# Optimization experiments

Measured on AMD Instinct MI355X. Metric: run time of the kernel, lower is better.

## Reference

```python
import jax, jax.numpy as jnp
import numpy as np

V, H, HALF, L, B = 32000, 512, 256, 1024, 64
LN_EPS = 1e-5
DELTA_EPS = 1e-6


def _forward(seq, embed, ff_w1, ff_b1, ff_w2, ff_b2, ln_g, ln_b,
             sem_w, sem_b, epi_w, epi_b, out_w, out_b):
    # Encoder: embed -> residual FFN -> LayerNorm
    e = embed[seq]                                   # (B, L, H)
    ff = jax.nn.relu(e @ ff_w1 + ff_b1) @ ff_w2 + ff_b2
    x = e + ff
    mu = jnp.mean(x, axis=-1, keepdims=True)
    var = jnp.mean((x - mu) ** 2, axis=-1, keepdims=True)
    h = (x - mu) / jnp.sqrt(var + LN_EPS) * ln_g + ln_b  # (B, L, H)

    # Project all timesteps at once (batched GEMM instead of per-step Linear)
    ks_all = h @ sem_w + sem_b                       # (B, L, half)
    ke_all = h @ epi_w + epi_b                       # (B, L, half)

    Bsz = seq.shape[0]
    Ls = seq.shape[1]
    w_t = jnp.arange(1, Ls, dtype=h.dtype) / Ls      # (L-1,) linear recency weights

    def step(carry, inp):
        M_s, M_e = carry
        k_s, k_e, w = inp                            # (B, half), (B, half), scalar
        vps = jnp.einsum('bij,bj->bi', M_s, k_s)
        dvs = k_s - vps / (jnp.sum(k_s * k_s, axis=-1, keepdims=True) + DELTA_EPS)
        M_s = M_s + dvs[:, :, None] * k_s[:, None, :]
        vpe = jnp.einsum('bij,bj->bi', M_e, k_e)
        dve = k_e - vpe / (jnp.sum(k_e * k_e, axis=-1, keepdims=True) + DELTA_EPS)
        M_e = M_e + w * (dve[:, :, None] * k_e[:, None, :])
        return (M_s, M_e), None

    M0 = jnp.zeros((Bsz, HALF, HALF), dtype=h.dtype)
    xs = (jnp.swapaxes(ks_all[:, :-1], 0, 1),        # (L-1, B, half)
          jnp.swapaxes(ke_all[:, :-1], 0, 1),
          w_t)
    (M_s, M_e), _ = jax.lax.scan(step, (M0, M0), xs)

    cs = jnp.einsum('bij,bj->bi', M_s, ks_all[:, -1])
    ce = jnp.einsum('bij,bj->bi', M_e, ke_all[:, -1])
    return jnp.concatenate([cs, ce], axis=-1) @ out_w + out_b  # (B, V)


def setup_inputs() -> dict:
    key = jax.random.key(0)
    ks = jax.random.split(key, 8)
    n = lambda k, shape, s=0.02: jax.random.normal(k, shape, jnp.float32) * s
    return {
        'seq': jax.random.randint(ks[0], (B, L), 0, V),
        'embed': n(ks[1], (V, H)),
        'ff_w1': n(ks[2], (H, 2 * H)), 'ff_b1': jnp.zeros((2 * H,), jnp.float32),
        'ff_w2': n(ks[3], (2 * H, H)), 'ff_b2': jnp.zeros((H,), jnp.float32),
        'ln_g': jnp.ones((H,), jnp.float32), 'ln_b': jnp.zeros((H,), jnp.float32),
        'sem_w': n(ks[4], (H, HALF)), 'sem_b': jnp.zeros((HALF,), jnp.float32),
        'epi_w': n(ks[5], (H, HALF)), 'epi_b': jnp.zeros((HALF,), jnp.float32),
        'out_w': n(ks[6], (2 * HALF, V)), 'out_b': jnp.zeros((V,), jnp.float32),
    }


def reference(seq, embed, ff_w1, ff_b1, ff_w2, ff_b2, ln_g, ln_b,
              sem_w, sem_b, epi_w, epi_b, out_w, out_b):
    return _forward(seq, embed, ff_w1, ff_b1, ff_w2, ff_b2, ln_g, ln_b,
                    sem_w, sem_b, epi_w, epi_b, out_w, out_b)
```

## Files before the change

### kernel.cpp

```cpp
#include <hip/hip_runtime.h>

typedef unsigned short ushort_t;
typedef unsigned int uint_t;
typedef __attribute__((ext_vector_type(8))) short short8;
typedef __attribute__((ext_vector_type(4))) float f32x4;

static constexpr int V = 32000, H = 512, HALFD = 256, LSEQ = 1024, BB = 64;

__device__ __forceinline__ ushort_t f2bf(float f) {
    uint_t u = __float_as_uint(f);
    u = (u + 0x7FFFu + ((u >> 16) & 1u)) >> 16;
    return (ushort_t)u;
}
__device__ __forceinline__ float bf2f(ushort_t u) {
    return __uint_as_float(((uint_t)u) << 16);
}
__device__ __forceinline__ float bflo(uint_t u) { return __uint_as_float(u << 16); }
__device__ __forceinline__ float bfhi(uint_t u) { return __uint_as_float(u & 0xffff0000u); }

__global__ void transpose_cvt(const float* __restrict__ W, ushort_t* __restrict__ Wt,
                              int K, int N) {
    __shared__ float tile[32][33];
    int k0 = blockIdx.y * 32, n0 = blockIdx.x * 32;
    int tx = threadIdx.x & 31, ty = threadIdx.x >> 5;
    #pragma unroll
    for (int i = 0; i < 32; i += 8)
        tile[ty + i][tx] = W[(size_t)(k0 + ty + i) * N + n0 + tx];
    __syncthreads();
    #pragma unroll
    for (int i = 0; i < 32; i += 8)
        Wt[(size_t)(n0 + ty + i) * K + k0 + tx] = f2bf(tile[tx][ty + i]);
}

__global__ __launch_bounds__(256) void gemm_ffn1(
        const int* __restrict__ seqp, const float* __restrict__ embed,
        const ushort_t* __restrict__ Bt, const float* __restrict__ bias,
        ushort_t* __restrict__ Cout, int N, int K) {
    __shared__ __align__(16) ushort_t Al[128][40];
    __shared__ __align__(16) ushort_t Bl[128][40];
    int t = threadIdx.x;
    int m0 = blockIdx.y * 128, n0 = blockIdx.x * 128;
    int lane = t & 63, wid = t >> 6;
    int wm = (wid & 1) * 64, wn = (wid >> 1) * 64;
    int lid = lane & 15, quad = lane >> 4;
    int srow = t >> 2, skq = (t & 3) * 8;

    int tok0 = seqp[m0 + srow];
    int tok1 = seqp[m0 + 64 + srow];
    const float* e0 = embed + (size_t)tok0 * H + skq;
    const float* e1 = embed + (size_t)tok1 * H + skq;

    f32x4 acc[4][4];
    #pragma unroll
    for (int i = 0; i < 4; ++i)
        #pragma unroll
        for (int j = 0; j < 4; ++j)
            acc[i][j] = (f32x4){0.f, 0.f, 0.f, 0.f};

    for (int k0 = 0; k0 < K; k0 += 32) {
        float4 ea0 = *(const float4*)(e0 + k0);
        float4 eb0 = *(const float4*)(e0 + k0 + 4);
        float4 ea1 = *(const float4*)(e1 + k0);
        float4 eb1 = *(const float4*)(e1 + k0 + 4);
        short8 b0 = *(const short8*)(Bt + (size_t)(n0 + srow) * K + k0 + skq);
        short8 b1 = *(const short8*)(Bt + (size_t)(n0 + 64 + srow) * K + k0 + skq);
        short8 s0, s1;
        s0[0] = (short)f2bf(ea0.x); s0[1] = (short)f2bf(ea0.y);
        s0[2] = (short)f2bf(ea0.z); s0[3] = (short)f2bf(ea0.w);
        s0[4] = (short)f2bf(eb0.x); s0[5] = (short)f2bf(eb0.y);
        s0[6] = (short)f2bf(eb0.z); s0[7] = (short)f2bf(eb0.w);
        s1[0] = (short)f2bf(ea1.x); s1[1] = (short)f2bf(ea1.y);
        s1[2] = (short)f2bf(ea1.z); s1[3] = (short)f2bf(ea1.w);
        s1[4] = (short)f2bf(eb1.x); s1[5] = (short)f2bf(eb1.y);
        s1[6] = (short)f2bf(eb1.z); s1[7] = (short)f2bf(eb1.w);
        __syncthreads();
        *(short8*)&Al[srow][skq]      = s0;
        *(short8*)&Al[64 + srow][skq] = s1;
        *(short8*)&Bl[srow][skq]      = b0;
        *(short8*)&Bl[64 + srow][skq] = b1;
        __syncthreads();
        short8 af[4], bfr[4];
        #pragma unroll
        for (int i = 0; i < 4; ++i)
            af[i] = *(const short8*)&Al[wm + i * 16 + lid][quad * 8];
        #pragma unroll
        for (int i = 0; i < 4; ++i)
            bfr[i] = *(const short8*)&Bl[wn + i * 16 + lid][quad * 8];
        #pragma unroll
        for (int mt = 0; mt < 4; ++mt)
            #pragma unroll
            for (int nt = 0; nt < 4; ++nt)
                acc[mt][nt] = __builtin_amdgcn_mfma_f32_16x16x32_bf16(
                    af[mt], bfr[nt], acc[mt][nt], 0, 0, 0);
    }
    #pragma unroll
    for (int mt = 0; mt < 4; ++mt)
        #pragma unroll
        for (int nt = 0; nt < 4; ++nt)
            #pragma unroll
            for (int rg = 0; rg < 4; ++rg) {
                int row = m0 + wm + mt * 16 + quad * 4 + rg;
                int col = n0 + wn + nt * 16 + lid;
                float v = fmaxf(acc[mt][nt][rg] + bias[col], 0.f);
                Cout[(size_t)row * N + col] = f2bf(v);
            }
}

__global__ __launch_bounds__(256) void gemm_ffn2(
        const ushort_t* __restrict__ A, const ushort_t* __restrict__ Bt,
        const float* __restrict__ bias, const int* __restrict__ seqp,
        const float* __restrict__ embed, ushort_t* __restrict__ Cout,
        int N, int K) {
    __shared__ __align__(16) ushort_t Al[128][40];
    __shared__ __align__(16) ushort_t Bl[128][40];
    int t = threadIdx.x;
    int m0 = blockIdx.y * 128, n0 = blockIdx.x * 128;
    int lane = t & 63, wid = t >> 6;
    int wm = (wid & 1) * 64, wn = (wid >> 1) * 64;
    int lid = lane & 15, quad = lane >> 4;
    int srow = t >> 2, skq = (t & 3) * 8;

    f32x4 acc[4][4];
    #pragma unroll
    for (int i = 0; i < 4; ++i)
        #pragma unroll
        for (int j = 0; j < 4; ++j)
            acc[i][j] = (f32x4){0.f, 0.f, 0.f, 0.f};

    for (int k0 = 0; k0 < K; k0 += 32) {
        short8 a0 = *(const short8*)(A + (size_t)(m0 + srow) * K + k0 + skq);
        short8 a1 = *(const short8*)(A + (size_t)(m0 + 64 + srow) * K + k0 + skq);
        short8 b0 = *(const short8*)(Bt + (size_t)(n0 + srow) * K + k0 + skq);
        short8 b1 = *(const short8*)(Bt + (size_t)(n0 + 64 + srow) * K + k0 + skq);
        __syncthreads();
        *(short8*)&Al[srow][skq]      = a0;
        *(short8*)&Al[64 + srow][skq] = a1;
        *(short8*)&Bl[srow][skq]      = b0;
        *(short8*)&Bl[64 + srow][skq] = b1;
        __syncthreads();
        short8 af[4], bfr[4];
        #pragma unroll
        for (int i = 0; i < 4; ++i)
            af[i] = *(const short8*)&Al[wm + i * 16 + lid][quad * 8];
        #pragma unroll
        for (int i = 0; i < 4; ++i)
            bfr[i] = *(const short8*)&Bl[wn + i * 16 + lid][quad * 8];
        #pragma unroll
        for (int mt = 0; mt < 4; ++mt)
            #pragma unroll
            for (int nt = 0; nt < 4; ++nt)
                acc[mt][nt] = __builtin_amdgcn_mfma_f32_16x16x32_bf16(
                    af[mt], bfr[nt], acc[mt][nt], 0, 0, 0);
    }
    #pragma unroll
    for (int mt = 0; mt < 4; ++mt)
        #pragma unroll
        for (int rg = 0; rg < 4; ++rg) {
            int row = m0 + wm + mt * 16 + quad * 4 + rg;
            int tok = seqp[row];
            const float* erow = embed + (size_t)tok * H;
            #pragma unroll
            for (int nt = 0; nt < 4; ++nt) {
                int col = n0 + wn + nt * 16 + lid;
                float v = acc[mt][nt][rg] + bias[col] + erow[col];
                Cout[(size_t)row * N + col] = f2bf(v);
            }
        }
}

__global__ __launch_bounds__(256) void gemm_proj(
        const ushort_t* __restrict__ A, const ushort_t* __restrict__ Bt,
        const float* __restrict__ biasS, const float* __restrict__ biasE,
        ushort_t* __restrict__ outS, ushort_t* __restrict__ outE, int K) {
    __shared__ __align__(16) ushort_t Al[128][40];
    __shared__ __align__(16) ushort_t Bl[128][40];
    int t = threadIdx.x;
    int m0 = blockIdx.y * 128, n0 = blockIdx.x * 128;
    int lane = t & 63, wid = t >> 6;
    int wm = (wid & 1) * 64, wn = (wid >> 1) * 64;
    int lid = lane & 15, quad = lane >> 4;
    int srow = t >> 2, skq = (t & 3) * 8;

    f32x4 acc[4][4];
    #pragma unroll
    for (int i = 0; i < 4; ++i)
        #pragma unroll
        for (int j = 0; j < 4; ++j)
            acc[i][j] = (f32x4){0.f, 0.f, 0.f, 0.f};

    for (int k0 = 0; k0 < K; k0 += 32) {
        short8 a0 = *(const short8*)(A + (size_t)(m0 + srow) * K + k0 + skq);
        short8 a1 = *(const short8*)(A + (size_t)(m0 + 64 + srow) * K + k0 + skq);
        short8 b0 = *(const short8*)(Bt + (size_t)(n0 + srow) * K + k0 + skq);
        short8 b1 = *(const short8*)(Bt + (size_t)(n0 + 64 + srow) * K + k0 + skq);
        __syncthreads();
        *(short8*)&Al[srow][skq]      = a0;
        *(short8*)&Al[64 + srow][skq] = a1;
        *(short8*)&Bl[srow][skq]      = b0;
        *(short8*)&Bl[64 + srow][skq] = b1;
        __syncthreads();
        short8 af[4], bfr[4];
        #pragma unroll
        for (int i = 0; i < 4; ++i)
            af[i] = *(const short8*)&Al[wm + i * 16 + lid][quad * 8];
        #pragma unroll
        for (int i = 0; i < 4; ++i)
            bfr[i] = *(const short8*)&Bl[wn + i * 16 + lid][quad * 8];
        #pragma unroll
        for (int mt = 0; mt < 4; ++mt)
            #pragma unroll
            for (int nt = 0; nt < 4; ++nt)
                acc[mt][nt] = __builtin_amdgcn_mfma_f32_16x16x32_bf16(
                    af[mt], bfr[nt], acc[mt][nt], 0, 0, 0);
    }
    #pragma unroll
    for (int mt = 0; mt < 4; ++mt)
        #pragma unroll
        for (int nt = 0; nt < 4; ++nt)
            #pragma unroll
            for (int rg = 0; rg < 4; ++rg) {
                int row = m0 + wm + mt * 16 + quad * 4 + rg;
                int col = n0 + wn + nt * 16 + lid;
                if (col < 256)
                    outS[(size_t)row * HALFD + col] = f2bf(acc[mt][nt][rg] + biasS[col]);
                else
                    outE[(size_t)row * HALFD + col - 256] =
                        f2bf(acc[mt][nt][rg] + biasE[col - 256]);
            }
}

__global__ void ln_kernel(ushort_t* X, const float* __restrict__ g,
                          const float* __restrict__ bta) {
    int row = blockIdx.x * 4 + (threadIdx.x >> 6);
    int lane = threadIdx.x & 63;
    ushort_t* xr = X + (size_t)row * H + lane * 8;
    short8 xv = *(short8*)xr;
    float x[8];
    #pragma unroll
    for (int j = 0; j < 8; ++j) x[j] = bf2f((ushort_t)xv[j]);
    float s = 0.f, ss = 0.f;
    #pragma unroll
    for (int j = 0; j < 8; ++j) { s += x[j]; ss += x[j] * x[j]; }
    #pragma unroll
    for (int d = 1; d < 64; d <<= 1) { s += __shfl_xor(s, d); ss += __shfl_xor(ss, d); }
    float mu = s * (1.f / 512.f);
    float var = ss * (1.f / 512.f) - mu * mu;
    float rstd = rsqrtf(var + 1e-5f);
    float4 g0 = *(const float4*)(g + lane * 8);
    float4 g1 = *(const float4*)(g + lane * 8 + 4);
    float4 b0 = *(const float4*)(bta + lane * 8);
    float4 b1 = *(const float4*)(bta + lane * 8 + 4);
    float gg[8] = {g0.x, g0.y, g0.z, g0.w, g1.x, g1.y, g1.z, g1.w};
    float bb[8] = {b0.x, b0.y, b0.z, b0.w, b1.x, b1.y, b1.z, b1.w};
    short8 o;
    #pragma unroll
    for (int j = 0; j < 8; ++j)
        o[j] = (short)f2bf((x[j] - mu) * rstd * gg[j] + bb[j]);
    *(short8*)xr = o;
}

__global__ void beta_kernel(const ushort_t* __restrict__ k, float* __restrict__ beta) {
    int row = blockIdx.x * 4 + (threadIdx.x >> 6);
    int lane = threadIdx.x & 63;
    ushort4 a = *(const ushort4*)(k + (size_t)row * HALFD + lane * 4);
    float ax = bf2f(a.x), ay = bf2f(a.y), az = bf2f(a.z), aw = bf2f(a.w);
    float s = ax * ax + ay * ay + az * az + aw * aw;
    #pragma unroll
    for (int d = 1; d < 64; d <<= 1) s += __shfl_xor(s, d);
    if (lane == 0) beta[row] = s + 1e-6f;
}

__global__ __launch_bounds__(256) void tinv_kernel(
        const ushort_t* __restrict__ ks, const ushort_t* __restrict__ ke,
        const float* __restrict__ beta_s, const float* __restrict__ beta_e,
        ushort_t* __restrict__ Dg) {
    int blk = blockIdx.x;
    int ch = blk & 15;
    int bm = blk >> 4;
    int mat = bm & 1, b = bm >> 1;
    const ushort_t* Kp = (mat ? ke : ks) + ((size_t)b * LSEQ + ch * 64) * HALFD;
    const float* Bp = (mat ? beta_e : beta_s) + (size_t)b * LSEQ + ch * 64;

    __shared__ __align__(16) ushort_t Kl[64][264];
    __shared__ float Lm[64][65];
    __shared__ float Drow[64];
    __shared__ float betsl[64];

    int t = threadIdx.x;
    int lane = t & 63, wv = t >> 6;
    int lid = lane & 15, quad = lane >> 4;

    {
        int j = t >> 2, c0 = (t & 3) * 64;
        const ushort_t* src = Kp + (size_t)j * HALFD + c0;
        #pragma unroll
        for (int x = 0; x < 8; ++x)
            *(short8*)&Kl[j][c0 + x * 8] = *(const short8*)(src + x * 8);
    }
    if (t < 64) betsl[t] = Bp[t];
    __syncthreads();

    f32x4 g[4];
    #pragma unroll
    for (int i = 0; i < 4; ++i) g[i] = (f32x4){0.f, 0.f, 0.f, 0.f};
    #pragma unroll
    for (int kc = 0; kc < 8; ++kc) {
        short8 af = *(const short8*)&Kl[wv * 16 + lid][kc * 32 + quad * 8];
        #pragma unroll
        for (int nt = 0; nt < 4; ++nt) {
            short8 bq = *(const short8*)&Kl[nt * 16 + lid][kc * 32 + quad * 8];
            g[nt] = __builtin_amdgcn_mfma_f32_16x16x32_bf16(af, bq, g[nt], 0, 0, 0);
        }
    }
    const float invL = 1.0f / 1024.0f;
    #pragma unroll
    for (int nt = 0; nt < 4; ++nt)
        #pragma unroll
        for (int rg = 0; rg < 4; ++rg) {
            int i = wv * 16 + quad * 4 + rg;
            int j = nt * 16 + lid;
            int s = ch * 64 + i;
            float wgt = mat ? (float)(s + 1) * invL : 1.0f;
            if (s >= 1023) wgt = 0.f;
            float wb = wgt / betsl[i];
            Lm[i][j] = (j < i) ? g[nt][rg] * wb : 0.f;
        }
    __syncthreads();

    float a[16];
    #pragma unroll
    for (int ii = 0; ii < 16; ++ii) a[ii] = -Lm[wv * 16 + ii][lane];
    #pragma unroll 63
    for (int j = 0; j < 63; ++j) {
        if (wv == (j >> 4)) Drow[lane] = a[j & 15];
        __syncthreads();
        float dj = Drow[lane];
        #pragma unroll
        for (int ii = 0; ii < 16; ++ii) {
            int i = wv * 16 + ii;
            if (i > j) a[ii] -= Lm[i][j] * dj;
        }
        __syncthreads();
    }
    #pragma unroll
    for (int ii = 0; ii < 16; ++ii)
        Dg[(size_t)blk * 4096 + (size_t)(wv * 16 + ii) * 64 + lane] = f2bf(a[ii]);
}

__global__ __launch_bounds__(512) void scan_kernel(
        const ushort_t* __restrict__ ks, const ushort_t* __restrict__ ke,
        const float* __restrict__ beta_s, const float* __restrict__ beta_e,
        const ushort_t* __restrict__ Dg, float* __restrict__ c) {
    int blk = blockIdx.x;
    int b = blk >> 2, mat = (blk >> 1) & 1, half = blk & 1;
    const ushort_t* Kp = (mat ? ke : ks) + (size_t)b * LSEQ * HALFD;
    const float* Bp = (mat ? beta_e : beta_s) + (size_t)b * LSEQ;
    const ushort_t* Dp = Dg + (size_t)(b * 2 + mat) * 16 * 4096;

    __shared__ __align__(16) ushort_t Kl[64][264];
    __shared__ __align__(16) ushort_t MK[33792];
    __shared__ __align__(16) ushort_t RHSl[128][72];
    __shared__ __align__(16) ushort_t Ul[128][72];
    __shared__ __align__(16) ushort_t Dl[64][72];
    __shared__ float bets[LSEQ];

    ushort_t (*Ml)[264] = (ushort_t(*)[264])MK;
    ushort_t (*Kt)[72]  = (ushort_t(*)[72])MK;

    int t = threadIdx.x;
    int lane = t & 63, wid = t >> 6;
    int lid = lane & 15, quad = lane >> 4;
    int wm  = (wid & 1) * 64, wn  = (wid >> 1) * 64;
    int wm1 = (wid & 1) * 64, wn1 = (wid >> 1) * 16;

    #pragma unroll
    for (int i = 0; i < 2; ++i) bets[t + i * 512] = Bp[t + i * 512];

    f32x4 acc[4][4];
    #pragma unroll
    for (int i = 0; i < 4; ++i)
        #pragma unroll
        for (int j = 0; j < 4; ++j)
            acc[i][j] = (f32x4){0.f, 0.f, 0.f, 0.f};

    int sj = t >> 3, scb = (t & 7) * 8;
    short8 pf[4];
    {
        const ushort_t* kr = Kp + (size_t)sj * HALFD + scb;
        #pragma unroll
        for (int x = 0; x < 4; ++x) pf[x] = *(const short8*)(kr + x * 64);
    }
    short8 dpf = *(const short8*)(Dp + t * 8);
    const float invL = 1.0f / 1024.0f;

    for (int ch = 0; ch < 16; ++ch) {
        __syncthreads();
        #pragma unroll
        for (int x = 0; x < 4; ++x) *(short8*)&Kl[sj][scb + x * 64] = pf[x];
        *(short8*)&Dl[t >> 3][(t & 7) * 8] = dpf;
        #pragma unroll
        for (int mt = 0; mt < 4; ++mt)
            #pragma unroll
            for (int nt = 0; nt < 4; ++nt)
                #pragma unroll
                for (int rg = 0; rg < 4; ++rg)
                    Ml[wm + mt * 16 + quad * 4 + rg][wn + nt * 16 + lid] =
                        f2bf(acc[mt][nt][rg]);
        int nch = (ch + 1 < 16) ? ch + 1 : 15;
        {
            const ushort_t* kr = Kp + ((size_t)nch * 64 + sj) * HALFD + scb;
            #pragma unroll
            for (int x = 0; x < 4; ++x) pf[x] = *(const short8*)(kr + x * 64);
            dpf = *(const short8*)(Dp + (size_t)nch * 4096 + t * 8);
        }
        __syncthreads();

        f32x4 p0[4];
        #pragma unroll
        for (int i = 0; i < 4; ++i) p0[i] = (f32x4){0.f, 0.f, 0.f, 0.f};
        #pragma unroll
        for (int kc = 0; kc < 8; ++kc) {
            short8 bq = *(const short8*)&Kl[wn1 + lid][kc * 32 + quad * 8];
            #pragma unroll
            for (int mt = 0; mt < 4; ++mt) {
                short8 aq = *(const short8*)&Ml[wm1 + mt * 16 + lid][kc * 32 + quad * 8];
                p0[mt] = __builtin_amdgcn_mfma_f32_16x16x32_bf16(aq, bq, p0[mt], 0, 0, 0);
            }
        }
        __syncthreads();
        #pragma unroll
        for (int mt = 0; mt < 4; ++mt)
            #pragma unroll
            for (int nt = 0; nt < 4; ++nt)
                #pragma unroll
                for (int rg = 0; rg < 4; ++rg) {
                    float v = acc[mt][nt][rg];
                    Ml[wm + mt * 16 + quad * 4 + rg][wn + nt * 16 + lid] =
                        f2bf(v - bf2f(f2bf(v)));
                }
        __syncthreads();
        #pragma unroll
        for (int kc = 0; kc < 8; ++kc) {
            short8 bq = *(const short8*)&Kl[wn1 + lid][kc * 32 + quad * 8];
            #pragma unroll
            for (int mt = 0; mt < 4; ++mt) {
                short8 aq = *(const short8*)&Ml[wm1 + mt * 16 + lid][kc * 32 + quad * 8];
                p0[mt] = __builtin_amdgcn_mfma_f32_16x16x32_bf16(aq, bq, p0[mt], 0, 0, 0);
            }
        }
        int iB = wn1 + lid;
        int s = ch * 64 + iB;
        float wgt = mat ? (float)(s + 1) * invL : 1.0f;
        if (s >= 1023) wgt = 0.f;
        float wb = wgt / bets[s];
        float rhsf[4][4];
        #pragma unroll
        for (int mt = 0; mt < 4; ++mt)
            #pragma unroll
            for (int rg = 0; rg < 4; ++rg) {
                int r = wm1 + mt * 16 + quad * 4 + rg;
                float kv = bf2f(Kl[iB][half * 128 + r]);
                float rv = wgt * kv - wb * p0[mt][rg];
                rhsf[mt][rg] = rv;
                RHSl[r][iB] = f2bf(rv);
            }
        __syncthreads();

        {
            int c0 = wid * 32;
            #pragma unroll
            for (int rr = 0; rr < 4; ++rr) {
                short8 kv8 = *(const short8*)&Kl[lane][c0 + rr * 8];
                #pragma unroll
                for (int x = 0; x < 8; ++x)
                    Kt[c0 + rr * 8 + x][lane] = (ushort_t)kv8[x];
            }
        }
        f32x4 uf[4];
        #pragma unroll
        for (int i = 0; i < 4; ++i) uf[i] = (f32x4){0.f, 0.f, 0.f, 0.f};
        #pragma unroll
        for (int kc = 0; kc < 2; ++kc) {
            short8 bq = *(const short8*)&Dl[wn1 + lid][kc * 32 + quad * 8];
            #pragma unroll
            for (int mt = 0; mt < 4; ++mt) {
                short8 aq = *(const short8*)&RHSl[wm1 + mt * 16 + lid][kc * 32 + quad * 8];
                uf[mt] = __builtin_amdgcn_mfma_f32_16x16x32_bf16(aq, bq, uf[mt], 0, 0, 0);
            }
        }
        #pragma unroll
        for (int mt = 0; mt < 4; ++mt)
            #pragma unroll
            for (int rg = 0; rg < 4; ++rg) {
                int r = wm1 + mt * 16 + quad * 4 + rg;
                Ul[r][wn1 + lid] = f2bf(uf[mt][rg] + rhsf[mt][rg]);
            }
        __syncthreads();
        #pragma unroll
        for (int kc = 0; kc < 2; ++kc) {
            short8 bq4[4];
            #pragma unroll
            for (int nt = 0; nt < 4; ++nt)
                bq4[nt] = *(const short8*)&Kt[wn + nt * 16 + lid][kc * 32 + quad * 8];
            #pragma unroll
            for (int mt = 0; mt < 4; ++mt) {
                short8 aq = *(const short8*)&Ul[wm + mt * 16 + lid][kc * 32 + quad * 8];
                #pragma unroll
                for (int nt = 0; nt < 4; ++nt)
                    acc[mt][nt] = __builtin_amdgcn_mfma_f32_16x16x32_bf16(
                        aq, bq4[nt], acc[mt][nt], 0, 0, 0);
            }
        }
        __syncthreads();
        #pragma unroll
        for (int mt = 0; mt < 4; ++mt)
            #pragma unroll
            for (int rg = 0; rg < 4; ++rg) {
                int r = wm1 + mt * 16 + quad * 4 + rg;
                float u = uf[mt][rg] + rhsf[mt][rg];
                Ul[r][wn1 + lid] = f2bf(u - bf2f(f2bf(u)));
            }
        __syncthreads();
        #pragma unroll
        for (int kc = 0; kc < 2; ++kc) {
            short8 bq4[4];
            #pragma unroll
            for (int nt = 0; nt < 4; ++nt)
                bq4[nt] = *(const short8*)&Kt[wn + nt * 16 + lid][kc * 32 + quad * 8];
            #pragma unroll
            for (int mt = 0; mt < 4; ++mt) {
                short8 aq = *(const short8*)&Ul[wm + mt * 16 + lid][kc * 32 + quad * 8];
                #pragma unroll
                for (int nt = 0; nt < 4; ++nt)
                    acc[mt][nt] = __builtin_amdgcn_mfma_f32_16x16x32_bf16(
                        aq, bq4[nt], acc[mt][nt], 0, 0, 0);
            }
        }
    }

    __syncthreads();
    float* vsc = (float*)RHSl;
    float kvv[4];
    #pragma unroll
    for (int nt = 0; nt < 4; ++nt)
        kvv[nt] = bf2f(Kl[63][wn + nt * 16 + lid]);
    #pragma unroll
    for (int mt = 0; mt < 4; ++mt)
        #pragma unroll
        for (int rg = 0; rg < 4; ++rg) {
            float p = acc[mt][0][rg] * kvv[0] + acc[mt][1][rg] * kvv[1]
                    + acc[mt][2][rg] * kvv[2] + acc[mt][3][rg] * kvv[3];
            p += __shfl_xor(p, 1); p += __shfl_xor(p, 2);
            p += __shfl_xor(p, 4); p += __shfl_xor(p, 8);
            if (lid == 0)
                vsc[(wid >> 1) * 128 + wm + mt * 16 + quad * 4 + rg] = p;
        }
    __syncthreads();
    if (t < 128) {
        float sum = vsc[t] + vsc[128 + t] + vsc[256 + t] + vsc[384 + t];
        c[(size_t)b * 512 + mat * 256 + half * 128 + t] = sum;
    }
}

__global__ __launch_bounds__(512) void out_gemm(
        const float* __restrict__ c, const float* __restrict__ W,
        const float* __restrict__ bias, float* __restrict__ out) {
    __shared__ __align__(16) float cl[16][512];
    int t = threadIdx.x;
    int lane = t & 63, w = t >> 6;
    int cb = blockIdx.x * 256;
    int rb = blockIdx.y * 16;

    #pragma unroll
    for (int i = 0; i < 4; ++i) {
        int idx = t + i * 512;
        int row = idx >> 7, c4 = (idx & 127) * 4;
        *(float4*)&cl[row][c4] = *(const float4*)(c + (size_t)(rb + row) * 512 + c4);
    }
    __syncthreads();

    const float* wp = W + cb + lane * 4;
    int r0 = w * 2;
    f32x4 a0 = (f32x4){0.f, 0.f, 0.f, 0.f};
    f32x4 a1 = (f32x4){0.f, 0.f, 0.f, 0.f};

    #pragma unroll 2
    for (int k = 0; k < 512; k += 4) {
        f32x4 w0 = *(const f32x4*)(wp + (size_t)(k + 0) * V);
        f32x4 w1 = *(const f32x4*)(wp + (size_t)(k + 1) * V);
        f32x4 w2 = *(const f32x4*)(wp + (size_t)(k + 2) * V);
        f32x4 w3 = *(const f32x4*)(wp + (size_t)(k + 3) * V);
        f32x4 ca = *(const f32x4*)&cl[r0][k];
        f32x4 cb4 = *(const f32x4*)&cl[r0 + 1][k];
        a0 += ca[0] * w0; a0 += ca[1] * w1; a0 += ca[2] * w2; a0 += ca[3] * w3;
        a1 += cb4[0] * w0; a1 += cb4[1] * w1; a1 += cb4[2] * w2; a1 += cb4[3] * w3;
    }
    f32x4 bv = *(const f32x4*)(bias + cb + lane * 4);
    *(f32x4*)(out + (size_t)(rb + r0) * V + cb + lane * 4) = a0 + bv;
    *(f32x4*)(out + (size_t)(rb + r0 + 1) * V + cb + lane * 4) = a1 + bv;
}

extern "C" void kernel_launch(void* const* d_in, const int* in_sizes, int n_in,
                              void* d_out, int out_size, void* d_ws, size_t ws_size,
                              hipStream_t stream) {
    const int*   seq    = (const int*)d_in[0];
    const float* embed  = (const float*)d_in[1];
    const float* ff_w1  = (const float*)d_in[2];
    const float* ff_b1  = (const float*)d_in[3];
    const float* ff_w2  = (const float*)d_in[4];
    const float* ff_b2  = (const float*)d_in[5];
    const float* ln_g   = (const float*)d_in[6];
    const float* ln_b   = (const float*)d_in[7];
    const float* sem_w  = (const float*)d_in[8];
    const float* sem_b  = (const float*)d_in[9];
    const float* epi_w  = (const float*)d_in[10];
    const float* epi_b  = (const float*)d_in[11];
    const float* out_w  = (const float*)d_in[12];
    const float* out_b  = (const float*)d_in[13];
    float* outp = (float*)d_out;

    const int ML = BB * LSEQ;
    int RCH;
    if      (ws_size >= 271712256ull) RCH = 65536;
    else if (ws_size >= 120717312ull) RCH = 16384;
    else                              RCH = 8192;

    char* w = (char*)d_ws;
    size_t off = 0;
    ushort_t* ks_bf = (ushort_t*)(w + off); off += 33554432;
    ushort_t* ke_bf = (ushort_t*)(w + off); off += 33554432;
    ushort_t* ebc   = (ushort_t*)(w + off); off += (size_t)RCH * 512 * 2;
    ushort_t* t1c   = (ushort_t*)(w + off); off += (size_t)RCH * 1024 * 2;
    ushort_t* w1t   = (ushort_t*)(w + off); off += 1048576;
    ushort_t* w2t   = (ushort_t*)(w + off); off += 1048576;
    ushort_t* semt  = (ushort_t*)(w + off); off += 262144;
    ushort_t* epit  = (ushort_t*)(w + off); off += 262144;
    float*    bet_s = (float*)(w + off);    off += 262144;
    float*    bet_e = (float*)(w + off);    off += 262144;
    float*    cbuf  = (float*)(w + off);    off += 131072;
    ushort_t* Dbuf  = ebc;
    (void)t1c;

    transpose_cvt<<<dim3(1024 / 32, 512 / 32), 256, 0, stream>>>(ff_w1, w1t, 512, 1024);
    transpose_cvt<<<dim3(512 / 32, 1024 / 32), 256, 0, stream>>>(ff_w2, w2t, 1024, 512);
    transpose_cvt<<<dim3(256 / 32, 512 / 32), 256, 0, stream>>>(sem_w, semt, 512, 256);
    transpose_cvt<<<dim3(256 / 32, 512 / 32), 256, 0, stream>>>(epi_w, epit, 512, 256);

    for (int cc = 0; cc < ML / RCH; ++cc) {
        int c0 = cc * RCH;
        gemm_ffn1<<<dim3(1024 / 128, RCH / 128), 256, 0, stream>>>(
            seq + c0, embed, w1t, ff_b1, t1c, 1024, 512);
        gemm_ffn2<<<dim3(512 / 128, RCH / 128), 256, 0, stream>>>(
            t1c, w2t, ff_b2, seq + c0, embed, ebc, 512, 1024);
        ln_kernel<<<RCH / 4, 256, 0, stream>>>(ebc, ln_g, ln_b);
        gemm_proj<<<dim3(512 / 128, RCH / 128), 256, 0, stream>>>(
            ebc, semt, sem_b, epi_b,
            ks_bf + (size_t)c0 * HALFD, ke_bf + (size_t)c0 * HALFD, 512);
    }

    beta_kernel<<<ML / 4, 256, 0, stream>>>(ks_bf, bet_s);
    beta_kernel<<<ML / 4, 256, 0, stream>>>(ke_bf, bet_e);

    tinv_kernel<<<2048, 256, 0, stream>>>(ks_bf, ke_bf, bet_s, bet_e, Dbuf);
    scan_kernel<<<256, 512, 0, stream>>>(ks_bf, ke_bf, bet_s, bet_e, Dbuf, cbuf);

    out_gemm<<<dim3(125, 4), 512, 0, stream>>>(cbuf, out_w, out_b, outp);
}
```

Measured before the change: 1.006 ms.

## Barrier-free per-wave triangular inverse and paired DPP bf16 LDS stores in scan

Measured after the change: 961.9 us. -4.4%, faster.

```diff
diff --git a/kernel.cpp b/kernel.cpp
--- a/kernel.cpp
+++ b/kernel.cpp
@@ -17,6 +17,21 @@
 }
 __device__ __forceinline__ float bflo(uint_t u) { return __uint_as_float(u << 16); }
 __device__ __forceinline__ float bfhi(uint_t u) { return __uint_as_float(u & 0xffff0000u); }
+__device__ __forceinline__ float bfres(float v) { return v - bf2f(f2bf(v)); }
+
+__device__ __forceinline__ uint_t dppswap1(uint_t x) {
+    return (uint_t)__builtin_amdgcn_mov_dpp((int)x, 0xB1, 0xF, 0xF, true);
+}
+
+__device__ __forceinline__ void st_pair4(ushort_t* p0, int pitch, int codd,
+                                         float v0, float v1, float v2, float v3) {
+    uint_t b0 = f2bf(v0), b1 = f2bf(v1), b2 = f2bf(v2), b3 = f2bf(v3);
+    uint_t q0 = dppswap1(b0), q1 = dppswap1(b1), q2 = dppswap1(b2), q3 = dppswap1(b3);
+    uint_t wa = codd ? ((uint_t)q2 | ((uint_t)b2 << 16)) : ((uint_t)b0 | ((uint_t)q0 << 16));
+    uint_t wb = codd ? ((uint_t)q3 | ((uint_t)b3 << 16)) : ((uint_t)b1 | ((uint_t)q1 << 16));
+    *(uint_t*)(p0) = wa;
+    *(uint_t*)(p0 + pitch) = wb;
+}
 
 __global__ void transpose_cvt(const float* __restrict__ W, ushort_t* __restrict__ Wt,
                               int K, int N) {
@@ -274,77 +289,84 @@
         const ushort_t* __restrict__ ks, const ushort_t* __restrict__ ke,
         const float* __restrict__ beta_s, const float* __restrict__ beta_e,
         ushort_t* __restrict__ Dg) {
-    int blk = blockIdx.x;
-    int ch = blk & 15;
-    int bm = blk >> 4;
-    int mat = bm & 1, b = bm >> 1;
-    const ushort_t* Kp = (mat ? ke : ks) + ((size_t)b * LSEQ + ch * 64) * HALFD;
-    const float* Bp = (mat ? beta_e : beta_s) + (size_t)b * LSEQ + ch * 64;
-
-    __shared__ __align__(16) ushort_t Kl[64][264];
-    __shared__ float Lm[64][65];
-    __shared__ float Drow[64];
-    __shared__ float betsl[64];
+    __shared__ __align__(16) ushort_t Kl[64][280];
+    __shared__ __align__(16) ushort_t LmT[4][64][66];
+    __shared__ float betsl[4][64];
 
     int t = threadIdx.x;
     int lane = t & 63, wv = t >> 6;
     int lid = lane & 15, quad = lane >> 4;
-
-    {
-        int j = t >> 2, c0 = (t & 3) * 64;
-        const ushort_t* src = Kp + (size_t)j * HALFD + c0;
-        #pragma unroll
-        for (int x = 0; x < 8; ++x)
-            *(short8*)&Kl[j][c0 + x * 8] = *(const short8*)(src + x * 8);
-    }
-    if (t < 64) betsl[t] = Bp[t];
+    int blk0 = blockIdx.x * 4;
+    const float invL = 1.0f / 1024.0f;
+
+    for (int pp = 0; pp < 4; ++pp) {
+        int p = blk0 + pp;
+        int ch = p & 15, bm = p >> 4;
+        int mat = bm & 1, b = bm >> 1;
+        const ushort_t* Kp = (mat ? ke : ks) + ((size_t)b * LSEQ + ch * 64) * HALFD;
+        const float* Bp = (mat ? beta_e : beta_s) + (size_t)b * LSEQ + ch * 64;
+
+        __syncthreads();
+        {
+            int j = t >> 2, c0 = (t & 3) * 64;
+            const ushort_t* src = Kp + (size_t)j * HALFD + c0;
+            #pragma unroll
+            for (int x = 0; x < 8; ++x)
+                *(short8*)&Kl[j][c0 + x * 8] = *(const short8*)(src + x * 8);
+        }
+        if (t < 64) betsl[pp][t] = Bp[t];
+        __syncthreads();
+
+        f32x4 g[4];
+        #pragma unroll
+        for (int i = 0; i < 4; ++i) g[i] = (f32x4){0.f, 0.f, 0.f, 0.f};
+        #pragma unroll
+        for (int kc = 0; kc < 8; ++kc) {
+            short8 af = *(const short8*)&Kl[wv * 16 + lid][kc * 32 + quad * 8];
+            #pragma unroll
+            for (int nt = 0; nt < 4; ++nt) {
+                short8 bq = *(const short8*)&Kl[nt * 16 + lid][kc * 32 + quad * 8];
+                g[nt] = __builtin_amdgcn_mfma_f32_16x16x32_bf16(af, bq, g[nt], 0, 0, 0);
+            }
+        }
+        #pragma unroll
+        for (int nt = 0; nt < 4; ++nt)
+            #pragma unroll
+            for (int rg = 0; rg < 4; ++rg) {
+                int i = wv * 16 + quad * 4 + rg;
+                int j = nt * 16 + lid;
+                int s = ch * 64 + i;
+                float wgt = mat ? (float)(s + 1) * invL : 1.0f;
+                if (s >= 1023) wgt = 0.f;
+                float wb = wgt / betsl[pp][i];
+                LmT[pp][j][i] = f2bf((j < i) ? g[nt][rg] * wb : 0.f);
+            }
+    }
     __syncthreads();
 
-    f32x4 g[4];
-    #pragma unroll
-    for (int i = 0; i < 4; ++i) g[i] = (f32x4){0.f, 0.f, 0.f, 0.f};
-    #pragma unroll
-    for (int kc = 0; kc < 8; ++kc) {
-        short8 af = *(const short8*)&Kl[wv * 16 + lid][kc * 32 + quad * 8];
-        #pragma unroll
-        for (int nt = 0; nt < 4; ++nt) {
-            short8 bq = *(const short8*)&Kl[nt * 16 + lid][kc * 32 + quad * 8];
-            g[nt] = __builtin_amdgcn_mfma_f32_16x16x32_bf16(af, bq, g[nt], 0, 0, 0);
-        }
-    }
-    const float invL = 1.0f / 1024.0f;
-    #pragma unroll
-    for (int nt = 0; nt < 4; ++nt)
-        #pragma unroll
-        for (int rg = 0; rg < 4; ++rg) {
-            int i = wv * 16 + quad * 4 + rg;
-            int j = nt * 16 + lid;
-            int s = ch * 64 + i;
-            float wgt = mat ? (float)(s + 1) * invL : 1.0f;
-            if (s >= 1023) wgt = 0.f;
-            float wb = wgt / betsl[i];
-            Lm[i][j] = (j < i) ? g[nt][rg] * wb : 0.f;
-        }
-    __syncthreads();
-
-    float a[16];
-    #pragma unroll
-    for (int ii = 0; ii < 16; ++ii) a[ii] = -Lm[wv * 16 + ii][lane];
-    #pragma unroll 63
+    const ushort_t (*Lp)[66] = LmT[wv];
+    float a[64];
+    #pragma unroll
+    for (int x = 0; x < 32; ++x) {
+        uint_t u = *(const uint_t*)&Lp[lane][x * 2];
+        a[x * 2]     = -bflo(u);
+        a[x * 2 + 1] = -bfhi(u);
+    }
+    #pragma unroll
     for (int j = 0; j < 63; ++j) {
-        if (wv == (j >> 4)) Drow[lane] = a[j & 15];
-        __syncthreads();
-        float dj = Drow[lane];
-        #pragma unroll
-        for (int ii = 0; ii < 16; ++ii) {
-            int i = wv * 16 + ii;
-            if (i > j) a[ii] -= Lm[i][j] * dj;
-        }
-        __syncthreads();
-    }
-    #pragma unroll
-    for (int ii = 0; ii < 16; ++ii)
-        Dg[(size_t)blk * 4096 + (size_t)(wv * 16 + ii) * 64 + lane] = f2bf(a[ii]);
+        float dj = a[j];
+        const ushort_t* rowj = Lp[j];
+        #pragma unroll
+        for (int ii = (j + 1) & ~1; ii < 64; ii += 2) {
+            uint_t u = *(const uint_t*)&rowj[ii];
+            if (ii > j) a[ii] -= bflo(u) * dj;
+            a[ii + 1]        -= bfhi(u) * dj;
+        }
+    }
+    size_t pbase = (size_t)(blk0 + wv) * 4096;
+    #pragma unroll
+    for (int i = 0; i < 64; ++i)
+        Dg[pbase + (size_t)i * 64 + lane] = f2bf(a[i]);
 }
 
 __global__ __launch_bounds__(512) void scan_kernel(
@@ -357,24 +379,22 @@
     const float* Bp = (mat ? beta_e : beta_s) + (size_t)b * LSEQ;
     const ushort_t* Dp = Dg + (size_t)(b * 2 + mat) * 16 * 4096;
 
-    __shared__ __align__(16) ushort_t Kl[64][264];
-    __shared__ __align__(16) ushort_t MK[33792];
-    __shared__ __align__(16) ushort_t RHSl[128][72];
-    __shared__ __align__(16) ushort_t Ul[128][72];
+    __shared__ __align__(16) ushort_t Kl[64][280];
+    __shared__ __align__(16) ushort_t MK[35840];
+    __shared__ __align__(16) ushort_t RHSl[128][88];
+    __shared__ __align__(16) ushort_t Ul[128][88];
     __shared__ __align__(16) ushort_t Dl[64][72];
-    __shared__ float bets[LSEQ];
-
-    ushort_t (*Ml)[264] = (ushort_t(*)[264])MK;
-    ushort_t (*Kt)[72]  = (ushort_t(*)[72])MK;
+    __shared__ float betc[64];
+
+    ushort_t (*Ml)[280] = (ushort_t(*)[280])MK;
+    ushort_t (*Kt)[88]  = (ushort_t(*)[88])MK;
 
     int t = threadIdx.x;
     int lane = t & 63, wid = t >> 6;
     int lid = lane & 15, quad = lane >> 4;
+    int codd = lid & 1, lid2 = lid & ~1;
     int wm  = (wid & 1) * 64, wn  = (wid >> 1) * 64;
     int wm1 = (wid & 1) * 64, wn1 = (wid >> 1) * 16;
-
-    #pragma unroll
-    for (int i = 0; i < 2; ++i) bets[t + i * 512] = Bp[t + i * 512];
 
     f32x4 acc[4][4];
     #pragma unroll
@@ -391,6 +411,7 @@
         for (int x = 0; x < 4; ++x) pf[x] = *(const short8*)(kr + x * 64);
     }
     short8 dpf = *(const short8*)(Dp + t * 8);
+    float bpf = (t < 64) ? Bp[t] : 0.f;
     const float invL = 1.0f / 1024.0f;
 
     for (int ch = 0; ch < 16; ++ch) {
@@ -398,20 +419,22 @@
         #pragma unroll
         for (int x = 0; x < 4; ++x) *(short8*)&Kl[sj][scb + x * 64] = pf[x];
         *(short8*)&Dl[t >> 3][(t & 7) * 8] = dpf;
-        #pragma unroll
-        for (int mt = 0; mt < 4; ++mt)
+        if (t < 64) betc[t] = bpf;
+        #pragma unroll
+        for (int mt = 0; mt < 4; ++mt) {
+            int rb = wm + mt * 16 + quad * 4 + codd * 2;
             #pragma unroll
             for (int nt = 0; nt < 4; ++nt)
-                #pragma unroll
-                for (int rg = 0; rg < 4; ++rg)
-                    Ml[wm + mt * 16 + quad * 4 + rg][wn + nt * 16 + lid] =
-                        f2bf(acc[mt][nt][rg]);
+                st_pair4(&Ml[rb][wn + nt * 16 + lid2], 280, codd,
+                         acc[mt][nt][0], acc[mt][nt][1], acc[mt][nt][2], acc[mt][nt][3]);
+        }
         int nch = (ch + 1 < 16) ? ch + 1 : 15;
         {
             const ushort_t* kr = Kp + ((size_t)nch * 64 + sj) * HALFD + scb;
             #pragma unroll
             for (int x = 0; x < 4; ++x) pf[x] = *(const short8*)(kr + x * 64);
             dpf = *(const short8*)(Dp + (size_t)nch * 4096 + t * 8);
+            if (t < 64) bpf = Bp[nch * 64 + t];
         }
         __syncthreads();
 
@@ -429,15 +452,14 @@
         }
         __syncthreads();
         #pragma unroll
-        for (int mt = 0; mt < 4; ++mt)
+        for (int mt = 0; mt < 4; ++mt) {
+            int rb = wm + mt * 16 + quad * 4 + codd * 2;
             #pragma unroll
             for (int nt = 0; nt < 4; ++nt)
-                #pragma unroll
-                for (int rg = 0; rg < 4; ++rg) {
-                    float v = acc[mt][nt][rg];
-                    Ml[wm + mt * 16 + quad * 4 + rg][wn + nt * 16 + lid] =
-                        f2bf(v - bf2f(f2bf(v)));
-                }
+                st_pair4(&Ml[rb][wn + nt * 16 + lid2], 280, codd,
+                         bfres(acc[mt][nt][0]), bfres(acc[mt][nt][1]),
+                         bfres(acc[mt][nt][2]), bfres(acc[mt][nt][3]));
+        }
         __syncthreads();
         #pragma unroll
         for (int kc = 0; kc < 8; ++kc) {
@@ -452,7 +474,7 @@
         int s = ch * 64 + iB;
         float wgt = mat ? (float)(s + 1) * invL : 1.0f;
         if (s >= 1023) wgt = 0.f;
-        float wb = wgt / bets[s];
+        float wb = wgt / betc[iB];
         float rhsf[4][4];
         #pragma unroll
         for (int mt = 0; mt < 4; ++mt)
@@ -460,10 +482,12 @@
             for (int rg = 0; rg < 4; ++rg) {
                 int r = wm1 + mt * 16 + quad * 4 + rg;
                 float kv = bf2f(Kl[iB][half * 128 + r]);
-                float rv = wgt * kv - wb * p0[mt][rg];
-                rhsf[mt][rg] = rv;
-                RHSl[r][iB] = f2bf(rv);
-            }
+                rhsf[mt][rg] = wgt * kv - wb * p0[mt][rg];
+            }
+        #pragma unroll
+        for (int mt = 0; mt < 4; ++mt)
+            st_pair4(&RHSl[wm1 + mt * 16 + quad * 4 + codd * 2][wn1 + lid2], 88, codd,
+                     rhsf[mt][0], rhsf[mt][1], rhsf[mt][2], rhsf[mt][3]);
         __syncthreads();
 
         {
@@ -490,11 +514,9 @@
         }
         #pragma unroll
         for (int mt = 0; mt < 4; ++mt)
-            #pragma unroll
-            for (int rg = 0; rg < 4; ++rg) {
-                int r = wm1 + mt * 16 + quad * 4 + rg;
-                Ul[r][wn1 + lid] = f2bf(uf[mt][rg] + rhsf[mt][rg]);
-            }
+            st_pair4(&Ul[wm1 + mt * 16 + quad * 4 + codd * 2][wn1 + lid2], 88, codd,
+                     uf[mt][0] + rhsf[mt][0], uf[mt][1] + rhsf[mt][1],
+                     uf[mt][2] + rhsf[mt][2], uf[mt][3] + rhsf[mt][3]);
         __syncthreads();
         #pragma unroll
         for (int kc = 0; kc < 2; ++kc) {
@@ -513,13 +535,12 @@
         }
         __syncthreads();
         #pragma unroll
-        for (int mt = 0; mt < 4; ++mt)
-            #pragma unroll
-            for (int rg = 0; rg < 4; ++rg) {
-                int r = wm1 + mt * 16 + quad * 4 + rg;
-                float u = uf[mt][rg] + rhsf[mt][rg];
-                Ul[r][wn1 + lid] = f2bf(u - bf2f(f2bf(u)));
-            }
+        for (int mt = 0; mt < 4; ++mt) {
+            float u0 = uf[mt][0] + rhsf[mt][0], u1 = uf[mt][1] + rhsf[mt][1];
+            float u2 = uf[mt][2] + rhsf[mt][2], u3 = uf[mt][3] + rhsf[mt][3];
+            st_pair4(&Ul[wm1 + mt * 16 + quad * 4 + codd * 2][wn1 + lid2], 88, codd,
+                     bfres(u0), bfres(u1), bfres(u2), bfres(u3));
+        }
         __syncthreads();
         #pragma unroll
         for (int kc = 0; kc < 2; ++kc) {
@@ -661,7 +682,7 @@
     beta_kernel<<<ML / 4, 256, 0, stream>>>(ks_bf, bet_s);
     beta_kernel<<<ML / 4, 256, 0, stream>>>(ke_bf, bet_e);
 
-    tinv_kernel<<<2048, 256, 0, stream>>>(ks_bf, ke_bf, bet_s, bet_e, Dbuf);
+    tinv_kernel<<<512, 256, 0, stream>>>(ks_bf, ke_bf, bet_s, bet_e, Dbuf);
     scan_kernel<<<256, 512, 0, stream>>>(ks_bf, ke_bf, bet_s, bet_e, Dbuf, cbuf);
 
     out_gemm<<<dim3(125, 4), 512, 0, stream>>>(cbuf, out_w, out_b, outp);
```
